# Kernel optimization log

Measured on AMD Instinct MI355X. Metric: run time of the kernel, lower is better.

## Reference

```python
import jax, jax.numpy as jnp
import numpy as np

MAXG = 8          # max adaptive sampling grid (boxes generated so ceil(roi_size) <= 8)
SCALE = 0.125     # spatial_scale / ds (ds = 1.0)


def setup_inputs() -> dict:
    key = jax.random.key(0)
    ks = jax.random.split(key, 12)
    bs, N, ch, H, W = 8, 128, 1280, 64, 64
    out_ch, inner = 1024, 5120
    z = jax.random.normal(ks[0], (bs, ch, H, W), jnp.float32)
    # boxes (x1, y1, x2, y2) in 512x512 image coords, sizes in [8, 64] px
    x1 = jax.random.uniform(ks[1], (bs, N), minval=0.0, maxval=448.0)
    y1 = jax.random.uniform(ks[2], (bs, N), minval=0.0, maxval=448.0)
    bw = jax.random.uniform(ks[3], (bs, N), minval=8.0, maxval=64.0)
    bh = jax.random.uniform(ks[4], (bs, N), minval=8.0, maxval=64.0)
    bboxes = jnp.stack([x1, y1, x1 + bw, y1 + bh], axis=-1)

    def lin(k, fan_in, shape):
        return jax.random.normal(k, shape, jnp.float32) * (1.0 / np.sqrt(fan_in))

    W1 = lin(ks[5], ch, (ch, inner)); b1 = jnp.zeros((inner,), jnp.float32)
    W2 = lin(ks[6], inner, (inner, out_ch)); b2 = jnp.zeros((out_ch,), jnp.float32)
    S1 = lin(ks[7], 2, (2, 64)); sb1 = jnp.zeros((64,), jnp.float32)
    S2 = lin(ks[8], 64, (64, 256)); sb2 = jnp.zeros((256,), jnp.float32)
    S3 = lin(ks[9], 256, (256, out_ch)); sb3 = jnp.zeros((out_ch,), jnp.float32)
    O = lin(ks[10], 2 * out_ch, (2 * out_ch, out_ch)); ob = jnp.zeros((out_ch,), jnp.float32)
    return dict(z=z, bboxes=bboxes, W1=W1, b1=b1, W2=W2, b2=b2,
                S1=S1, sb1=sb1, S2=S2, sb2=sb2, S3=S3, sb3=sb3, O=O, ob=ob)


def _prep(c, size):
    # torchvision bilinear border handling for one coordinate axis
    oob = (c < -1.0) | (c > size)
    cc = jnp.clip(c, 0.0, None)
    lo0 = jnp.floor(cc)
    hi_case = lo0 >= size - 1
    lo = jnp.minimum(lo0, size - 1).astype(jnp.int32)
    hi = jnp.minimum(lo0 + 1, size - 1).astype(jnp.int32)
    frac = jnp.where(hi_case, 0.0, cc - lo0)
    return lo, hi, frac, oob


def _roi_align_1x1(z, bboxes):
    # torchvision roi_align, output_size=1, aligned=True, sampling_ratio=-1
    bs, ch, H, W = z.shape
    N = bboxes.shape[1]
    boxes = jax.lax.stop_gradient(bboxes).reshape(-1, 4) * SCALE - 0.5  # aligned
    bidx = jnp.repeat(jnp.arange(bs), N)
    rw = boxes[:, 2] - boxes[:, 0]
    rh = boxes[:, 3] - boxes[:, 1]
    gw = jnp.clip(jnp.ceil(rw), 1, MAXG)   # adaptive grid: ceil(roi_size / 1)
    gh = jnp.clip(jnp.ceil(rh), 1, MAXG)
    count = gh * gw
    i = jnp.arange(MAXG, dtype=jnp.float32)
    ys = boxes[:, 1:2] + (i[None] + 0.5) * rh[:, None] / gh[:, None]  # [R, G]
    xs = boxes[:, 0:1] + (i[None] + 0.5) * rw[:, None] / gw[:, None]
    vy = i[None] < gh[:, None]
    vx = i[None] < gw[:, None]
    yl, yh, fy, oy = _prep(ys, H)
    xl, xh, fx, ox = _prep(xs, W)
    my = (vy & ~oy).astype(z.dtype)
    mx = (vx & ~ox).astype(z.dtype)
    mask = my[:, :, None] * mx[:, None, :]             # [R, G, G]
    hy, ly = 1.0 - fy, fy
    hx, lx = 1.0 - fx, fx
    zt = jnp.transpose(z, (0, 2, 3, 1))                # [bs, H, W, ch]
    acc = jnp.zeros((bs * N, ch), z.dtype)
    corners = [(yl, xl, hy, hx), (yl, xh, hy, lx), (yh, xl, ly, hx), (yh, xh, ly, lx)]
    for yi, xi, wy, wx in corners:
        wt = mask * (wy[:, :, None] * wx[:, None, :])  # [R, G, G]
        v = zt[bidx[:, None, None], yi[:, :, None], xi[:, None, :]]  # [R, G, G, ch]
        acc = acc + jnp.einsum('rgh,rghc->rc', wt, v)
    return (acc / count[:, None]).reshape(bs, N, ch)


def reference(z, bboxes, W1, b1, W2, b2, S1, sb1, S2, sb2, S3, sb3, O, ob):
    x = _roi_align_1x1(z, bboxes)                      # [bs, N, ch]
    x = jax.nn.relu(x @ W1 + b1) @ W2 + b2             # out MLP
    # BBoxSizeEmbedder: (h, w) = (y2 - y1, x2 - x1)
    sz = jnp.stack([bboxes[..., 3] - bboxes[..., 1],
                    bboxes[..., 2] - bboxes[..., 0]], axis=-1)
    e = jax.nn.relu(sz @ S1 + sb1)
    e = jax.nn.relu(e @ S2 + sb2)
    e = e @ S3 + sb3
    return jnp.concatenate([x, e], axis=-1) @ O + ob   # out2
```

## Files before the change

### kernel.cpp

```cpp
#include <hip/hip_runtime.h>

static constexpr int kBS    = 8;
static constexpr int kNROI  = 128;
static constexpr int kR     = kBS * kNROI;
static constexpr int kCH    = 1280;
static constexpr int kH     = 64;
static constexpr int kW     = 64;
static constexpr int kPIX   = kH * kW;
static constexpr int kINNER = 5120;
static constexpr int kOUTC  = 1024;
static constexpr int kXE    = 2 * kOUTC;
static constexpr int kE2    = 256;

typedef _Float16 half8 __attribute__((ext_vector_type(8)));
typedef float floatx4 __attribute__((ext_vector_type(4)));

__device__ __forceinline__ void gload_lds16(const _Float16* g, _Float16* l) {
    __builtin_amdgcn_global_load_lds(
        (const __attribute__((address_space(1))) void*)g,
        (__attribute__((address_space(3))) void*)l,
        16, 0, 0);
}

static constexpr int kPC = 2;
static constexpr int kPS = 4100;
static constexpr int kFGat = (kCH / kPC) * kBS;
static constexpr int kFMlp = kFGat + 256;
static constexpr int kFAll = kFMlp + 13824;

__global__ __launch_bounds__(256) void front_all(const float* __restrict__ z,
                                                 const float* __restrict__ bboxes,
                                                 const float* __restrict__ W1,
                                                 const float* __restrict__ W2,
                                                 const float* __restrict__ O,
                                                 const float* __restrict__ S3,
                                                 _Float16* __restrict__ W1t,
                                                 _Float16* __restrict__ W2t,
                                                 _Float16* __restrict__ Ot,
                                                 _Float16* __restrict__ S3t,
                                                 const float* __restrict__ S1,
                                                 const float* __restrict__ sb1,
                                                 const float* __restrict__ S2,
                                                 const float* __restrict__ sb2,
                                                 _Float16* __restrict__ h2f,
                                                 _Float16* __restrict__ x) {
    __shared__ float smem[kPC * kPS + 12 * 128 + 12 * 128 + 512];
    const int bid = blockIdx.x;
    const int t   = threadIdx.x;

    if (bid < kFGat) {
        float* pl  = smem;
        float* ywL = smem + kPC * kPS;
        float* xwL = ywL + 12 * 128;
        int*   im  = (int*)(xwL + 12 * 128);
        const int b   = bid & 7;
        const int chg = bid >> 3;
        const int c0  = chg * kPC;
        const float* zb = z + ((size_t)b * kCH + c0) * kPIX;
#pragma unroll
        for (int i = 0; i < 8; ++i) {
            const int idx = t + i * 256;
            const int ch  = idx >> 10;
            const int w4  = (idx & 1023) * 4;
            const float4 v = *(const float4*)&zb[(size_t)ch * kPIX + w4];
            *(float4*)&pl[ch * kPS + w4] = v;
        }
        if (t < 128) {
            const int r = b * kNROI + t;
#pragma unroll
            for (int i = 0; i < 12; ++i) { ywL[i * 128 + t] = 0.0f; xwL[i * 128 + t] = 0.0f; }
            const float x1 = bboxes[r * 4 + 0] * 0.125f - 0.5f;
            const float y1 = bboxes[r * 4 + 1] * 0.125f - 0.5f;
            const float x2 = bboxes[r * 4 + 2] * 0.125f - 0.5f;
            const float y2 = bboxes[r * 4 + 3] * 0.125f - 0.5f;
            const float rw = x2 - x1, rh = y2 - y1;
            const float gwf = fminf(fmaxf(ceilf(rw), 1.0f), 8.0f);
            const float ghf = fminf(fmaxf(ceilf(rh), 1.0f), 8.0f);
            const int gw = (int)gwf, gh = (int)ghf;
            const float ic = 1.0f / (gwf * ghf);

            int ymin = 0, last = 0;
            for (int g = 0; g < gh; ++g) {
                const float c   = y1 + ((float)g + 0.5f) * rh / ghf;
                const bool oob  = (c < -1.0f) || (c > 64.0f);
                const float cc  = fmaxf(c, 0.0f);
                const float lo0 = floorf(cc);
                const bool hic  = (lo0 >= 63.0f);
                const int lo    = (int)fminf(lo0, 63.0f);
                const int hi    = (int)fminf(lo0 + 1.0f, 63.0f);
                const float fr  = hic ? 0.0f : (cc - lo0);
                const float m   = oob ? 0.0f : 1.0f;
                if (g == 0) ymin = lo;
                const int il = min(lo - ymin, 11);
                const int ih = min(hi - ymin, 11);
                ywL[il * 128 + t] += m * (1.0f - fr);
                ywL[ih * 128 + t] += m * fr;
                last = hi;
            }
            const int nyd = min(last - ymin + 1, 12);

            int xmin = 0; last = 0;
            for (int g = 0; g < gw; ++g) {
                const float c   = x1 + ((float)g + 0.5f) * rw / gwf;
                const bool oob  = (c < -1.0f) || (c > 64.0f);
                const float cc  = fmaxf(c, 0.0f);
                const float lo0 = floorf(cc);
                const bool hic  = (lo0 >= 63.0f);
                const int lo    = (int)fminf(lo0, 63.0f);
                const int hi    = (int)fminf(lo0 + 1.0f, 63.0f);
                const float fr  = hic ? 0.0f : (cc - lo0);
                const float m   = oob ? 0.0f : 1.0f;
                if (g == 0) xmin = lo;
                const int il = min(lo - xmin, 11);
                const int ih = min(hi - xmin, 11);
                xwL[il * 128 + t] += m * (1.0f - fr);
                xwL[ih * 128 + t] += m * fr;
                last = hi;
            }
            const int nxd = min(last - xmin + 1, 12);
#pragma unroll
            for (int i = 0; i < 12; ++i) ywL[i * 128 + t] *= ic;
            im[t] = ymin; im[128 + t] = xmin; im[256 + t] = nyd; im[384 + t] = nxd;
        }
        __syncthreads();
        const int ch = t & 1;
        const int ri = t >> 1;
        const int r  = b * kNROI + ri;
        const float* plc = pl + ch * kPS;
        const int ym = im[ri], xm = im[128 + ri];
        const int ny = im[256 + ri], nx = im[384 + ri];
        float acc = 0.0f;
        for (int iy = 0; iy < ny; ++iy) {
            const float wy = ywL[iy * 128 + ri];
            const int ro   = (ym + iy) * kW + xm;
            for (int ix = 0; ix < nx; ++ix)
                acc += wy * xwL[ix * 128 + ri] * plc[ro + ix];
        }
        x[(size_t)r * kCH + c0 + ch] = (_Float16)acc;
    } else if (bid < kFMlp) {
        const int r0 = (bid - kFGat) * 4;
        float* sz = smem;
        float* h1 = smem + 8;
        if (t < 8) {
            const int row = t >> 1;
            const int c   = t & 1;
            const float* bb = bboxes + (size_t)(r0 + row) * 4;
            sz[row * 2 + c] = (c == 0) ? (bb[3] - bb[1]) : (bb[2] - bb[0]);
        }
        __syncthreads();
        {
            const int row = t >> 6;
            const int j   = t & 63;
            const float v = sz[row * 2] * S1[j] + sz[row * 2 + 1] * S1[64 + j] + sb1[j];
            h1[row * 64 + j] = fmaxf(v, 0.0f);
        }
        __syncthreads();
        {
            float acc[4];
            const float b = sb2[t];
#pragma unroll
            for (int row = 0; row < 4; ++row) acc[row] = b;
#pragma unroll 16
            for (int k = 0; k < 64; ++k) {
                const float w = S2[k * 256 + t];
#pragma unroll
                for (int row = 0; row < 4; ++row) acc[row] += h1[row * 64 + k] * w;
            }
#pragma unroll
            for (int row = 0; row < 4; ++row)
                h2f[(size_t)(r0 + row) * kE2 + t] = (_Float16)fmaxf(acc[row], 0.0f);
        }
    } else {
        const int cb = bid - kFMlp;
        const float* W; _Float16* Wt; int K, N, tile;
        if (cb < 6400)        { W = W1; Wt = W1t; K = kCH;    N = kINNER; tile = cb; }
        else if (cb < 11520)  { W = W2; Wt = W2t; K = kINNER; N = kOUTC;  tile = cb - 6400; }
        else if (cb < 13568)  { W = O;  Wt = Ot;  K = kXE;    N = kOUTC;  tile = cb - 11520; }
        else                  { W = S3; Wt = S3t; K = kE2;    N = kOUTC;  tile = cb - 13568; }
        const int nt = N / 32;
        const int n0 = (tile % nt) * 32;
        const int k0 = (tile / nt) * 32;
        {
            const int row = t >> 3;
            const int c4  = (t & 7) * 4;
            const float4 v = *(const float4*)&W[(size_t)(k0 + row) * N + n0 + c4];
            float* tl = smem + row * 33 + c4;
            tl[0] = v.x; tl[1] = v.y; tl[2] = v.z; tl[3] = v.w;
        }
        __syncthreads();
        {
            const int n  = t >> 3;
            const int k4 = (t & 7) * 4;
            union { _Float16 h[4]; uint2 u; } pk;
#pragma unroll
            for (int j = 0; j < 4; ++j) pk.h[j] = (_Float16)smem[(k4 + j) * 33 + n];
            *(uint2*)&Wt[(size_t)(n0 + n) * K + k0 + k4] = pk.u;
        }
    }
}

template <int NSPLIT>
__global__ __launch_bounds__(256) void gemm_f16_sk(const _Float16* __restrict__ A,
                                                   const _Float16* __restrict__ Bt,
                                                   float* __restrict__ P,
                                                   int Kfull) {
    __shared__ _Float16 As[2][128 * 32];
    __shared__ _Float16 Bs[2][128 * 32];
    const int t    = threadIdx.x;
    const int lane = t & 63;
    const int wave = t >> 6;
    const int m0 = blockIdx.y * 128, n0 = blockIdx.x * 128;
    const int Ksplit = Kfull / NSPLIT;
    const int s  = blockIdx.z;
    const int Nn = gridDim.x * 128;
    const int Mm = gridDim.y * 128;

    const int c0 = t, c1 = t + 256;
    const _Float16* Ag0 = A + (size_t)(m0 + (c0 >> 2)) * Kfull + (c0 & 3) * 8 + s * Ksplit;
    const _Float16* Ag1 = A + (size_t)(m0 + (c1 >> 2)) * Kfull + (c1 & 3) * 8 + s * Ksplit;
    const _Float16* Bg0 = Bt + (size_t)(n0 + (c0 >> 2)) * Kfull + (c0 & 3) * 8 + s * Ksplit;
    const _Float16* Bg1 = Bt + (size_t)(n0 + (c1 >> 2)) * Kfull + (c1 & 3) * 8 + s * Ksplit;

    const int wm = (wave >> 1) * 64;
    const int wn = (wave & 1) * 64;
    const int fm = lane & 15;
    const int kq = (lane >> 4) * 8;

    floatx4 acc[4][4];
#pragma unroll
    for (int i = 0; i < 4; ++i)
#pragma unroll
        for (int j = 0; j < 4; ++j) acc[i][j] = (floatx4){0.f, 0.f, 0.f, 0.f};

    const int nsteps = Ksplit / 32;
    gload_lds16(Ag0, &As[0][c0 * 8]);
    gload_lds16(Ag1, &As[0][c1 * 8]);
    gload_lds16(Bg0, &Bs[0][c0 * 8]);
    gload_lds16(Bg1, &Bs[0][c1 * 8]);
    __syncthreads();

    for (int ks = 0; ks < nsteps; ++ks) {
        const int cur = ks & 1;
        if (ks + 1 < nsteps) {
            const int kn = (ks + 1) * 32;
            gload_lds16(Ag0 + kn, &As[cur ^ 1][c0 * 8]);
            gload_lds16(Ag1 + kn, &As[cur ^ 1][c1 * 8]);
            gload_lds16(Bg0 + kn, &Bs[cur ^ 1][c0 * 8]);
            gload_lds16(Bg1 + kn, &Bs[cur ^ 1][c1 * 8]);
        }
        half8 af[4], bfv[4];
#pragma unroll
        for (int i = 0; i < 4; ++i)
            af[i] = *(const half8*)&As[cur][(wm + i * 16 + fm) * 32 + kq];
#pragma unroll
        for (int j = 0; j < 4; ++j)
            bfv[j] = *(const half8*)&Bs[cur][(wn + j * 16 + fm) * 32 + kq];
#pragma unroll
        for (int i = 0; i < 4; ++i)
#pragma unroll
            for (int j = 0; j < 4; ++j)
                acc[i][j] = __builtin_amdgcn_mfma_f32_16x16x32_f16(af[i], bfv[j], acc[i][j], 0, 0, 0);
        __syncthreads();
    }

    float* Pp = P + (size_t)s * Mm * Nn;
    const int qr = (lane >> 4) * 4;
#pragma unroll
    for (int j = 0; j < 4; ++j) {
        const int col = n0 + wn + j * 16 + fm;
#pragma unroll
        for (int i = 0; i < 4; ++i) {
            const int row = m0 + wm + i * 16 + qr;
#pragma unroll
            for (int rr = 0; rr < 4; ++rr)
                Pp[(size_t)(row + rr) * Nn + col] = acc[i][j][rr];
        }
    }
}

__global__ __launch_bounds__(256) void gemm_dual(const _Float16* __restrict__ h2f,
                                                 const _Float16* __restrict__ S3t,
                                                 const float* __restrict__ sb3,
                                                 _Float16* __restrict__ xeR,
                                                 const _Float16* __restrict__ x,
                                                 const _Float16* __restrict__ W1t,
                                                 const float* __restrict__ b1,
                                                 _Float16* __restrict__ h) {
    __shared__ _Float16 As[2][128 * 32];
    __shared__ _Float16 Bs[2][128 * 32];
    const int bid = blockIdx.x;
    const _Float16* A; const _Float16* Bt; const float* bias; _Float16* Out;
    int Kfull, ldc, nbn, tile; bool relu;
    if (bid < 64) {
        A = h2f; Bt = S3t; bias = sb3; Out = xeR;
        Kfull = kE2; ldc = kXE; relu = false; nbn = kOUTC / 128; tile = bid;
    } else {
        A = x; Bt = W1t; bias = b1; Out = h;
        Kfull = kCH; ldc = kINNER; relu = true; nbn = kINNER / 128; tile = bid - 64;
    }
    const int n0 = (tile % nbn) * 128;
    const int m0 = (tile / nbn) * 128;

    const int t    = threadIdx.x;
    const int lane = t & 63;
    const int wave = t >> 6;

    const int c0 = t, c1 = t + 256;
    const _Float16* Ag0 = A + (size_t)(m0 + (c0 >> 2)) * Kfull + (c0 & 3) * 8;
    const _Float16* Ag1 = A + (size_t)(m0 + (c1 >> 2)) * Kfull + (c1 & 3) * 8;
    const _Float16* Bg0 = Bt + (size_t)(n0 + (c0 >> 2)) * Kfull + (c0 & 3) * 8;
    const _Float16* Bg1 = Bt + (size_t)(n0 + (c1 >> 2)) * Kfull + (c1 & 3) * 8;

    const int wm = (wave >> 1) * 64;
    const int wn = (wave & 1) * 64;
    const int fm = lane & 15;
    const int kq = (lane >> 4) * 8;

    floatx4 acc[4][4];
#pragma unroll
    for (int i = 0; i < 4; ++i)
#pragma unroll
        for (int j = 0; j < 4; ++j) acc[i][j] = (floatx4){0.f, 0.f, 0.f, 0.f};

    const int nsteps = Kfull / 32;
    gload_lds16(Ag0, &As[0][c0 * 8]);
    gload_lds16(Ag1, &As[0][c1 * 8]);
    gload_lds16(Bg0, &Bs[0][c0 * 8]);
    gload_lds16(Bg1, &Bs[0][c1 * 8]);
    __syncthreads();

    for (int ks = 0; ks < nsteps; ++ks) {
        const int cur = ks & 1;
        if (ks + 1 < nsteps) {
            const int kn = (ks + 1) * 32;
            gload_lds16(Ag0 + kn, &As[cur ^ 1][c0 * 8]);
            gload_lds16(Ag1 + kn, &As[cur ^ 1][c1 * 8]);
            gload_lds16(Bg0 + kn, &Bs[cur ^ 1][c0 * 8]);
            gload_lds16(Bg1 + kn, &Bs[cur ^ 1][c1 * 8]);
        }
        half8 af[4], bfv[4];
#pragma unroll
        for (int i = 0; i < 4; ++i)
            af[i] = *(const half8*)&As[cur][(wm + i * 16 + fm) * 32 + kq];
#pragma unroll
        for (int j = 0; j < 4; ++j)
            bfv[j] = *(const half8*)&Bs[cur][(wn + j * 16 + fm) * 32 + kq];
#pragma unroll
        for (int i = 0; i < 4; ++i)
#pragma unroll
            for (int j = 0; j < 4; ++j)
                acc[i][j] = __builtin_amdgcn_mfma_f32_16x16x32_f16(af[i], bfv[j], acc[i][j], 0, 0, 0);
        __syncthreads();
    }

    const int qr = (lane >> 4) * 4;
#pragma unroll
    for (int j = 0; j < 4; ++j) {
        const int col = n0 + wn + j * 16 + fm;
        const float bv = bias[col];
#pragma unroll
        for (int i = 0; i < 4; ++i) {
            const int row = m0 + wm + i * 16 + qr;
#pragma unroll
            for (int rr = 0; rr < 4; ++rr) {
                float v = acc[i][j][rr] + bv;
                if (relu) v = fmaxf(v, 0.f);
                Out[(size_t)(row + rr) * ldc + col] = (_Float16)v;
            }
        }
    }
}

template <bool RELU, bool F16OUT, int NSPLIT>
__global__ __launch_bounds__(256) void reduce_splitk(const float* __restrict__ P,
                                                     const float* __restrict__ bias,
                                                     void* __restrict__ Cout,
                                                     int Nn, int ldc) {
    const size_t idx = ((size_t)blockIdx.x * 256 + threadIdx.x) * 4;
    const size_t MN  = (size_t)gridDim.x * 1024;
    const int m = (int)(idx / (size_t)Nn);
    const int n = (int)(idx % (size_t)Nn);
    float4 acc = *(const float4*)(P + idx);
#pragma unroll
    for (int s = 1; s < NSPLIT; ++s) {
        const float4 v = *(const float4*)(P + (size_t)s * MN + idx);
        acc.x += v.x; acc.y += v.y; acc.z += v.z; acc.w += v.w;
    }
    const float4 b4 = *(const float4*)(bias + n);
    acc.x += b4.x; acc.y += b4.y; acc.z += b4.z; acc.w += b4.w;
    if (RELU) {
        acc.x = fmaxf(acc.x, 0.f); acc.y = fmaxf(acc.y, 0.f);
        acc.z = fmaxf(acc.z, 0.f); acc.w = fmaxf(acc.w, 0.f);
    }
    if (F16OUT) {
        union { _Float16 h[4]; uint2 u; } pk;
        pk.h[0] = (_Float16)acc.x; pk.h[1] = (_Float16)acc.y;
        pk.h[2] = (_Float16)acc.z; pk.h[3] = (_Float16)acc.w;
        *(uint2*)((_Float16*)Cout + (size_t)m * ldc + n) = pk.u;
    } else {
        *(float4*)((float*)Cout + (size_t)m * ldc + n) = acc;
    }
}

extern "C" void kernel_launch(void* const* d_in, const int* in_sizes, int n_in,
                              void* d_out, int out_size, void* d_ws, size_t ws_size,
                              hipStream_t stream) {
    (void)in_sizes; (void)n_in; (void)out_size; (void)ws_size;
    const float* z   = (const float*)d_in[0];
    const float* bb  = (const float*)d_in[1];
    const float* W1  = (const float*)d_in[2];
    const float* b1  = (const float*)d_in[3];
    const float* W2  = (const float*)d_in[4];
    const float* b2  = (const float*)d_in[5];
    const float* S1  = (const float*)d_in[6];
    const float* sb1 = (const float*)d_in[7];
    const float* S2  = (const float*)d_in[8];
    const float* sb2 = (const float*)d_in[9];
    const float* S3  = (const float*)d_in[10];
    const float* sb3 = (const float*)d_in[11];
    const float* O   = (const float*)d_in[12];
    const float* ob  = (const float*)d_in[13];
    float* out = (float*)d_out;

    char* ws = (char*)d_ws;
    size_t off = 0;
    auto alloc = [&](size_t bytes) {
        void* p = ws + off;
        off += (bytes + 255) & ~(size_t)255;
        return p;
    };
    _Float16* x    = (_Float16*)alloc((size_t)kR * kCH * 2);
    _Float16* h    = (_Float16*)alloc((size_t)kR * kINNER * 2);
    _Float16* xe   = (_Float16*)alloc((size_t)kR * kXE * 2);
    _Float16* W1t  = (_Float16*)alloc((size_t)kINNER * kCH * 2);
    _Float16* W2t  = (_Float16*)alloc((size_t)kOUTC * kINNER * 2);
    _Float16* Ot   = (_Float16*)alloc((size_t)kOUTC * kXE * 2);
    _Float16* S3t  = (_Float16*)alloc((size_t)kOUTC * kE2 * 2);
    _Float16* h2f  = (_Float16*)alloc((size_t)kR * kE2 * 2);
    float*    P    = (float*)alloc((size_t)8 * kR * kOUTC * 4);

    hipLaunchKernelGGL(front_all, dim3(kFAll), dim3(256), 0, stream,
                       z, bb, W1, W2, O, S3, W1t, W2t, Ot, S3t,
                       S1, sb1, S2, sb2, h2f, x);

    hipLaunchKernelGGL(gemm_dual, dim3(64 + (kINNER / 128) * (kR / 128)), dim3(256), 0,
                       stream, h2f, S3t, sb3, xe + kOUTC, x, W1t, b1, h);

    hipLaunchKernelGGL((gemm_f16_sk<8>), dim3(kOUTC / 128, kR / 128, 8), dim3(256), 0,
                       stream, h, W2t, P, kINNER);
    hipLaunchKernelGGL((reduce_splitk<false, true, 8>),
                       dim3((size_t)kR * kOUTC / 1024), dim3(256), 0, stream,
                       P, b2, xe, kOUTC, kXE);

    hipLaunchKernelGGL((gemm_f16_sk<8>), dim3(kOUTC / 128, kR / 128, 8), dim3(256), 0,
                       stream, xe, Ot, P, kXE);
    hipLaunchKernelGGL((reduce_splitk<false, false, 8>),
                       dim3((size_t)kR * kOUTC / 1024), dim3(256), 0, stream,
                       P, ob, out, kOUTC, kOUTC);
}
```

Before: 398.0 us.

## Interleave gather and weight-transpose blocks, store gathered planes as fp16 in LDS

The front kernel now interleaves its block types: every third block does the RoI gather and the others do weight transposes, with the size-MLP blocks moved to the end. This is meant to mix memory-heavy gather blocks with transpose blocks across the grid instead of running them in separate phases. The feature-map planes staged in LDS are converted to fp16, which cuts shared memory per block to about 30 KB and should let more gather blocks stay resident at once. The cost is an extra rounding of z to fp16 before bilinear interpolation, which slightly lowers precision.

```diff
diff --git a/kernel.cpp b/kernel.cpp
--- a/kernel.cpp
+++ b/kernel.cpp
@@ -22,11 +22,9 @@
         16, 0, 0);
 }
 
-static constexpr int kPC = 2;
-static constexpr int kPS = 4100;
-static constexpr int kFGat = (kCH / kPC) * kBS;
-static constexpr int kFMlp = kFGat + 256;
-static constexpr int kFAll = kFMlp + 13824;
+static constexpr int kPC  = 2;
+static constexpr int kPSh = 4104;
+static constexpr int kFAll = 19200;
 
 __global__ __launch_bounds__(256) void front_all(const float* __restrict__ z,
                                                  const float* __restrict__ bboxes,
@@ -44,17 +42,25 @@
                                                  const float* __restrict__ sb2,
                                                  _Float16* __restrict__ h2f,
                                                  _Float16* __restrict__ x) {
-    __shared__ float smem[kPC * kPS + 12 * 128 + 12 * 128 + 512];
+    __shared__ __align__(16) char smemRaw[30752];
     const int bid = blockIdx.x;
     const int t   = threadIdx.x;
 
-    if (bid < kFGat) {
-        float* pl  = smem;
-        float* ywL = smem + kPC * kPS;
+    int gid = -1, oid = -1;
+    if (bid < 15360) {
+        if (bid % 3 == 0) gid = bid / 3;
+        else              oid = (bid / 3) * 2 + (bid % 3) - 1;
+    } else {
+        oid = 10240 + (bid - 15360);
+    }
+
+    if (gid >= 0) {
+        _Float16* pl = (_Float16*)smemRaw;
+        float* ywL = (float*)(smemRaw + 16416);
         float* xwL = ywL + 12 * 128;
         int*   im  = (int*)(xwL + 12 * 128);
-        const int b   = bid & 7;
-        const int chg = bid >> 3;
+        const int b   = gid & 7;
+        const int chg = gid >> 3;
         const int c0  = chg * kPC;
         const float* zb = z + ((size_t)b * kCH + c0) * kPIX;
 #pragma unroll
@@ -63,7 +69,10 @@
             const int ch  = idx >> 10;
             const int w4  = (idx & 1023) * 4;
             const float4 v = *(const float4*)&zb[(size_t)ch * kPIX + w4];
-            *(float4*)&pl[ch * kPS + w4] = v;
+            union { _Float16 h[4]; uint2 u; } pk;
+            pk.h[0] = (_Float16)v.x; pk.h[1] = (_Float16)v.y;
+            pk.h[2] = (_Float16)v.z; pk.h[3] = (_Float16)v.w;
+            *(uint2*)&pl[ch * kPSh + w4] = pk.u;
         }
         if (t < 128) {
             const int r = b * kNROI + t;
@@ -126,7 +135,7 @@
         const int ch = t & 1;
         const int ri = t >> 1;
         const int r  = b * kNROI + ri;
-        const float* plc = pl + ch * kPS;
+        const _Float16* plc = pl + ch * kPSh;
         const int ym = im[ri], xm = im[128 + ri];
         const int ny = im[256 + ri], nx = im[384 + ri];
         float acc = 0.0f;
@@ -134,49 +143,16 @@
             const float wy = ywL[iy * 128 + ri];
             const int ro   = (ym + iy) * kW + xm;
             for (int ix = 0; ix < nx; ++ix)
-                acc += wy * xwL[ix * 128 + ri] * plc[ro + ix];
+                acc += wy * xwL[ix * 128 + ri] * (float)plc[ro + ix];
         }
         x[(size_t)r * kCH + c0 + ch] = (_Float16)acc;
-    } else if (bid < kFMlp) {
-        const int r0 = (bid - kFGat) * 4;
-        float* sz = smem;
-        float* h1 = smem + 8;
-        if (t < 8) {
-            const int row = t >> 1;
-            const int c   = t & 1;
-            const float* bb = bboxes + (size_t)(r0 + row) * 4;
-            sz[row * 2 + c] = (c == 0) ? (bb[3] - bb[1]) : (bb[2] - bb[0]);
-        }
-        __syncthreads();
-        {
-            const int row = t >> 6;
-            const int j   = t & 63;
-            const float v = sz[row * 2] * S1[j] + sz[row * 2 + 1] * S1[64 + j] + sb1[j];
-            h1[row * 64 + j] = fmaxf(v, 0.0f);
-        }
-        __syncthreads();
-        {
-            float acc[4];
-            const float b = sb2[t];
-#pragma unroll
-            for (int row = 0; row < 4; ++row) acc[row] = b;
-#pragma unroll 16
-            for (int k = 0; k < 64; ++k) {
-                const float w = S2[k * 256 + t];
-#pragma unroll
-                for (int row = 0; row < 4; ++row) acc[row] += h1[row * 64 + k] * w;
-            }
-#pragma unroll
-            for (int row = 0; row < 4; ++row)
-                h2f[(size_t)(r0 + row) * kE2 + t] = (_Float16)fmaxf(acc[row], 0.0f);
-        }
-    } else {
-        const int cb = bid - kFMlp;
+    } else if (oid < 13824) {
+        float* tileb = (float*)smemRaw;
         const float* W; _Float16* Wt; int K, N, tile;
-        if (cb < 6400)        { W = W1; Wt = W1t; K = kCH;    N = kINNER; tile = cb; }
-        else if (cb < 11520)  { W = W2; Wt = W2t; K = kINNER; N = kOUTC;  tile = cb - 6400; }
-        else if (cb < 13568)  { W = O;  Wt = Ot;  K = kXE;    N = kOUTC;  tile = cb - 11520; }
-        else                  { W = S3; Wt = S3t; K = kE2;    N = kOUTC;  tile = cb - 13568; }
+        if (oid < 6400)        { W = W1; Wt = W1t; K = kCH;    N = kINNER; tile = oid; }
+        else if (oid < 11520)  { W = W2; Wt = W2t; K = kINNER; N = kOUTC;  tile = oid - 6400; }
+        else if (oid < 13568)  { W = O;  Wt = Ot;  K = kXE;    N = kOUTC;  tile = oid - 11520; }
+        else                   { W = S3; Wt = S3t; K = kE2;    N = kOUTC;  tile = oid - 13568; }
         const int nt = N / 32;
         const int n0 = (tile % nt) * 32;
         const int k0 = (tile / nt) * 32;
@@ -184,7 +160,7 @@
             const int row = t >> 3;
             const int c4  = (t & 7) * 4;
             const float4 v = *(const float4*)&W[(size_t)(k0 + row) * N + n0 + c4];
-            float* tl = smem + row * 33 + c4;
+            float* tl = tileb + row * 33 + c4;
             tl[0] = v.x; tl[1] = v.y; tl[2] = v.z; tl[3] = v.w;
         }
         __syncthreads();
@@ -193,8 +169,41 @@
             const int k4 = (t & 7) * 4;
             union { _Float16 h[4]; uint2 u; } pk;
 #pragma unroll
-            for (int j = 0; j < 4; ++j) pk.h[j] = (_Float16)smem[(k4 + j) * 33 + n];
+            for (int j = 0; j < 4; ++j) pk.h[j] = (_Float16)tileb[(k4 + j) * 33 + n];
             *(uint2*)&Wt[(size_t)(n0 + n) * K + k0 + k4] = pk.u;
+        }
+    } else {
+        const int r0 = (oid - 13824) * 4;
+        float* sz = (float*)smemRaw;
+        float* h1 = (float*)smemRaw + 8;
+        if (t < 8) {
+            const int row = t >> 1;
+            const int c   = t & 1;
+            const float* bb = bboxes + (size_t)(r0 + row) * 4;
+            sz[row * 2 + c] = (c == 0) ? (bb[3] - bb[1]) : (bb[2] - bb[0]);
+        }
+        __syncthreads();
+        {
+            const int row = t >> 6;
+            const int j   = t & 63;
+            const float v = sz[row * 2] * S1[j] + sz[row * 2 + 1] * S1[64 + j] + sb1[j];
+            h1[row * 64 + j] = fmaxf(v, 0.0f);
+        }
+        __syncthreads();
+        {
+            float acc[4];
+            const float b = sb2[t];
+#pragma unroll
+            for (int row = 0; row < 4; ++row) acc[row] = b;
+#pragma unroll 16
+            for (int k = 0; k < 64; ++k) {
+                const float w = S2[k * 256 + t];
+#pragma unroll
+                for (int row = 0; row < 4; ++row) acc[row] += h1[row * 64 + k] * w;
+            }
+#pragma unroll
+            for (int row = 0; row < 4; ++row)
+                h2f[(size_t)(r0 + row) * kE2 + t] = (_Float16)fmaxf(acc[row], 0.0f);
         }
     }
 }
```

Measured after the change: 384.6 us. 1.03x faster.
